# Performance work log

Measured on AMD Instinct MI355X. Metric: run time of the kernel, lower is better.

## Reference

```python
import jax, jax.numpy as jnp
import numpy as np

O = 128      # o_size
E = 512      # embed_dim
H = 128      # h_size
V = 34       # num_letter
B = 2048     # batch
T = 512      # listener timesteps
EPS = 1e-5   # BatchNorm eps


def _lstm_cell(x, h, c, W_ih, W_hh, b_ih, b_hh):
    # PyTorch LSTMCell: gates ordered i, f, g, o
    g = x @ W_ih.T + b_ih + h @ W_hh.T + b_hh
    i, f, gg, o = jnp.split(g, 4, axis=1)
    c_new = jax.nn.sigmoid(f) * c + jax.nn.sigmoid(i) * jnp.tanh(gg)
    h_new = jax.nn.sigmoid(o) * jnp.tanh(c_new)
    return h_new, c_new


def setup_inputs() -> dict:
    key = jax.random.key(0)
    ks = jax.random.split(key, 32)
    d = {}
    d['hk'] = jax.random.normal(ks[0], (B, T, O), jnp.float32)
    d['hv'] = jax.random.normal(ks[1], (B, T, O), jnp.float32)
    d['y_1'] = jax.random.normal(ks[2], (B, E), jnp.float32)
    d['c_1'] = jax.random.normal(ks[3], (B, O), jnp.float32)
    d['sh_1'] = jax.random.normal(ks[4], (3, B, O), jnp.float32)
    d['sc_1'] = jax.random.normal(ks[5], (3, B, O), jnp.float32)
    d['mask'] = jnp.ones((B, T), jnp.float32)
    s = 0.05
    in_dims = [O + E, O, O]
    for l in range(3):
        d[f'W_ih{l}'] = jax.random.normal(ks[6 + 4 * l], (4 * O, in_dims[l]), jnp.float32) * s
        d[f'W_hh{l}'] = jax.random.normal(ks[7 + 4 * l], (4 * O, O), jnp.float32) * s
        d[f'b_ih{l}'] = jax.random.normal(ks[8 + 4 * l], (4 * O,), jnp.float32) * s
        d[f'b_hh{l}'] = jax.random.normal(ks[9 + 4 * l], (4 * O,), jnp.float32) * s
    d['w1'] = jax.random.normal(ks[20], (H, O), jnp.float32) * s
    d['b1'] = jnp.zeros((H,), jnp.float32)
    d['w2'] = jax.random.normal(ks[21], (H, O), jnp.float32) * s
    d['b2'] = jnp.zeros((H,), jnp.float32)
    d['w3'] = jax.random.normal(ks[22], (V, H), jnp.float32) * s
    d['b3'] = jnp.zeros((V,), jnp.float32)
    d['gamma'] = jnp.ones((H,), jnp.float32)
    d['beta'] = jnp.zeros((H,), jnp.float32)
    return d


def reference(hk, hv, y_1, c_1, sh_1, sc_1, mask,
              W_ih0, W_hh0, b_ih0, b_hh0,
              W_ih1, W_hh1, b_ih1, b_hh1,
              W_ih2, W_hh2, b_ih2, b_hh2,
              w1, b1, w2, b2, w3, b3, gamma, beta):
    x0 = jnp.concatenate((y_1, c_1), axis=1)            # [B, E+O]
    sh0, sc0 = _lstm_cell(x0, sh_1[0], sc_1[0], W_ih0, W_hh0, b_ih0, b_hh0)
    sh1, sc1 = _lstm_cell(sh0, sh_1[1], sc_1[1], W_ih1, W_hh1, b_ih1, b_hh1)
    sh2, sc2 = _lstm_cell(sh1, sh_1[2], sc_1[2], W_ih2, W_hh2, b_ih2, b_hh2)

    # Attention: query is the CELL state sc2 (as in the original code)
    scores = jnp.einsum('bto,bo->bt', hk, sc2)           # [B, T]
    p = jax.nn.softmax(scores, axis=1)
    p = p * mask
    p = p / jnp.sum(p, axis=1, keepdims=True)            # mask-then-renormalize
    c = jnp.einsum('bt,bto->bo', p, hv)                  # [B, O]

    out = sh2 @ w1.T + b1 + (c @ w2.T + b2)              # [B, H]
    # BatchNorm1d (training mode: batch statistics, biased variance)
    mu = jnp.mean(out, axis=0)
    var = jnp.mean((out - mu) ** 2, axis=0)
    out = gamma * (out - mu) * jax.lax.rsqrt(var + EPS) + beta
    out = jax.nn.relu(out)
    out = out @ w3.T + b3                                # [B, V]
    out = jax.nn.softmax(out, axis=1)
    return out, c, jnp.stack([sh0, sh1, sh2]), jnp.stack([sc0, sc1, sc2])
```

## Files before the change

### kernel.cpp

```cpp
#include <hip/hip_runtime.h>
#include <hip/hip_bf16.h>

#define BSZ 2048
#define TSZ 512
#define OSZ 128
#define ESZ 512
#define HSZ 128
#define VSZ 34

#define OFF_C   69632
#define OFF_SH  331776
#define OFF_SC  1118208
#define LAYER   262144

__device__ __forceinline__ float sigf(float x)  { return 1.0f / (1.0f + __expf(-x)); }
__device__ __forceinline__ float tanhf_(float x){ return 2.0f / (1.0f + __expf(-2.0f * x)) - 1.0f; }

__global__ __launch_bounds__(256) void lstm_cell_kernel(
    const float* __restrict__ A0, int w0,
    const float* __restrict__ A1, int w1,
    const float* __restrict__ A2,
    const float* __restrict__ Wih, int in_dim,
    const float* __restrict__ Whh,
    const float* __restrict__ bih, const float* __restrict__ bhh,
    const float* __restrict__ c_prev,
    float* __restrict__ h_out, float* __restrict__ c_out,
    int K)
{
    __shared__ float As[16][68];
    __shared__ float Bs[16][68];

    const int tid = threadIdx.x;
    const int bm = blockIdx.x * 64;
    const int bn = blockIdx.y * 64;

    const int lRow = tid >> 2;
    const int lKq  = (tid & 3) * 4;

    const int nPerm = bn + (tid >> 2);
    const int nSrc  = (nPerm & 3) * 128 + (nPerm >> 2);

    const int tx = tid & 15, ty = tid >> 4;
    const int jT = (bn >> 2) + tx;

    float acc[4][4];
#pragma unroll
    for (int cc = 0; cc < 4; ++cc) {
        float bv = bih[cc * 128 + jT] + bhh[cc * 128 + jT];
#pragma unroll
        for (int r = 0; r < 4; ++r) acc[r][cc] = bv;
    }

    auto loadA = [&](int k0) -> float4 {
        int kg = k0 + lKq;
        const float* p;
        if (kg < w0)           p = A0 + (size_t)(bm + lRow) * w0 + kg;
        else if (kg < w0 + w1) p = A1 + (size_t)(bm + lRow) * w1 + (kg - w0);
        else                   p = A2 + (size_t)(bm + lRow) * 128 + (kg - w0 - w1);
        return *(const float4*)p;
    };
    auto loadB = [&](int k0) -> float4 {
        int kg = k0 + lKq;
        const float* p;
        if (kg < in_dim) p = Wih + (size_t)nSrc * in_dim + kg;
        else             p = Whh + (size_t)nSrc * 128 + (kg - in_dim);
        return *(const float4*)p;
    };

    float4 aR = loadA(0);
    float4 bR = loadB(0);
    const int ktiles = K >> 4;

    for (int kt = 0; kt < ktiles; ++kt) {
        As[lKq + 0][lRow] = aR.x; As[lKq + 1][lRow] = aR.y;
        As[lKq + 2][lRow] = aR.z; As[lKq + 3][lRow] = aR.w;
        Bs[lKq + 0][tid >> 2] = bR.x; Bs[lKq + 1][tid >> 2] = bR.y;
        Bs[lKq + 2][tid >> 2] = bR.z; Bs[lKq + 3][tid >> 2] = bR.w;
        __syncthreads();
        if (kt + 1 < ktiles) {
            aR = loadA((kt + 1) << 4);
            bR = loadB((kt + 1) << 4);
        }
#pragma unroll
        for (int k = 0; k < 16; ++k) {
            float4 av = *(const float4*)&As[k][ty * 4];
            float4 bv = *(const float4*)&Bs[k][tx * 4];
            float a_[4] = {av.x, av.y, av.z, av.w};
            float b_[4] = {bv.x, bv.y, bv.z, bv.w};
#pragma unroll
            for (int r = 0; r < 4; ++r)
#pragma unroll
                for (int c = 0; c < 4; ++c)
                    acc[r][c] += a_[r] * b_[c];
        }
        __syncthreads();
    }

#pragma unroll
    for (int r = 0; r < 4; ++r) {
        int row = bm + ty * 4 + r;
        float gi = acc[r][0], gf = acc[r][1], gg = acc[r][2], go = acc[r][3];
        float cp = c_prev[(size_t)row * 128 + jT];
        float cn = sigf(gf) * cp + sigf(gi) * tanhf_(gg);
        float hn = sigf(go) * tanhf_(cn);
        c_out[(size_t)row * 128 + jT] = cn;
        h_out[(size_t)row * 128 + jT] = hn;
    }
}

__global__ __launch_bounds__(256) void attn_kernel(
    const float* __restrict__ hk, const float* __restrict__ hv,
    const float* __restrict__ mask, const float* __restrict__ sc2,
    float* __restrict__ c_out)
{
    const int b = blockIdx.x;
    const int tid = threadIdx.x;
    __shared__ float sP[512];
    __shared__ float sRed[8];
    __shared__ float sC[8][128];

    const float* hkb = hk + (size_t)b * (TSZ * OSZ);
    const int og = (tid & 31) * 4;
    const int tg = tid >> 5;
    float4 q = *(const float4*)(sc2 + (size_t)b * 128 + og);

    for (int it = 0; it < 64; ++it) {
        float4 v = *(const float4*)(hkb + it * 1024 + tid * 4);
        float d = v.x * q.x + v.y * q.y + v.z * q.z + v.w * q.w;
        d += __shfl_xor(d, 1, 32);
        d += __shfl_xor(d, 2, 32);
        d += __shfl_xor(d, 4, 32);
        d += __shfl_xor(d, 8, 32);
        d += __shfl_xor(d, 16, 32);
        if ((tid & 31) == 0) sP[it * 8 + tg] = d;
    }
    __syncthreads();

    float m = fmaxf(sP[tid], sP[tid + 256]);
#pragma unroll
    for (int off = 1; off < 64; off <<= 1) m = fmaxf(m, __shfl_xor(m, off, 64));
    if ((tid & 63) == 0) sRed[tid >> 6] = m;
    __syncthreads();
    m = fmaxf(fmaxf(sRed[0], sRed[1]), fmaxf(sRed[2], sRed[3]));

    const float* mk = mask + (size_t)b * TSZ;
    float e0 = __expf(sP[tid] - m) * mk[tid];
    float e1 = __expf(sP[tid + 256] - m) * mk[tid + 256];
    float s = e0 + e1;
#pragma unroll
    for (int off = 1; off < 64; off <<= 1) s += __shfl_xor(s, off, 64);
    if ((tid & 63) == 0) sRed[4 + (tid >> 6)] = s;
    __syncthreads();
    float inv = 1.0f / (sRed[4] + sRed[5] + sRed[6] + sRed[7]);
    sP[tid]       = e0 * inv;
    sP[tid + 256] = e1 * inv;
    __syncthreads();

    float4 acc = {0.f, 0.f, 0.f, 0.f};
    const float* hvb = hv + (size_t)b * (TSZ * OSZ);
    for (int it = 0; it < 64; ++it) {
        float p = sP[it * 8 + tg];
        float4 v = *(const float4*)(hvb + it * 1024 + tid * 4);
        acc.x += p * v.x; acc.y += p * v.y; acc.z += p * v.z; acc.w += p * v.w;
    }
    *(float4*)&sC[tg][og] = acc;
    __syncthreads();
    if (tid < 128) {
        float r = 0.f;
#pragma unroll
        for (int g = 0; g < 8; ++g) r += sC[g][tid];
        c_out[(size_t)b * 128 + tid] = r;
    }
}

__global__ __launch_bounds__(256) void head_pre_kernel(
    const float* __restrict__ sh2, const float* __restrict__ cvec,
    const float* __restrict__ w1, const float* __restrict__ b1,
    const float* __restrict__ w2, const float* __restrict__ b2,
    float* __restrict__ out_pre, float* __restrict__ sum_part,
    float* __restrict__ sq_part)
{
    __shared__ float xs[8][128];
    __shared__ float xc[8][128];
    __shared__ float ps[2][128];
    __shared__ float pq[2][128];
    const int tid = threadIdx.x;
    const int rb = blockIdx.x * 8;
    {
        int row = tid >> 5, off = (tid & 31) * 4;
        *(float4*)&xs[row][off] = *(const float4*)(sh2 + (size_t)(rb + row) * 128 + off);
        *(float4*)&xc[row][off] = *(const float4*)(cvec + (size_t)(rb + row) * 128 + off);
    }
    __syncthreads();

    const int col = tid & 127, rg = tid >> 7;
    float acc[4];
    float bb = b1[col] + b2[col];
#pragma unroll
    for (int r = 0; r < 4; ++r) acc[r] = bb;
    const float* w1r = w1 + (size_t)col * 128;
    const float* w2r = w2 + (size_t)col * 128;
    for (int k4 = 0; k4 < 32; ++k4) {
        float4 wa = *(const float4*)(w1r + k4 * 4);
        float4 wb = *(const float4*)(w2r + k4 * 4);
#pragma unroll
        for (int r = 0; r < 4; ++r) {
            float4 xa = *(const float4*)&xs[rg * 4 + r][k4 * 4];
            float4 xb = *(const float4*)&xc[rg * 4 + r][k4 * 4];
            acc[r] += xa.x * wa.x + xa.y * wa.y + xa.z * wa.z + xa.w * wa.w
                    + xb.x * wb.x + xb.y * wb.y + xb.z * wb.z + xb.w * wb.w;
        }
    }
    float s = 0.f, q = 0.f;
#pragma unroll
    for (int r = 0; r < 4; ++r) {
        out_pre[(size_t)(rb + rg * 4 + r) * 128 + col] = acc[r];
        s += acc[r]; q += acc[r] * acc[r];
    }
    ps[rg][col] = s; pq[rg][col] = q;
    __syncthreads();
    if (rg == 0) {
        sum_part[blockIdx.x * 128 + col] = ps[0][col] + ps[1][col];
        sq_part[blockIdx.x * 128 + col]  = pq[0][col] + pq[1][col];
    }
}

__global__ __launch_bounds__(256) void bn_stats_kernel(
    const float* __restrict__ sum_part, const float* __restrict__ sq_part,
    float* __restrict__ mu_out, float* __restrict__ rstd_out)
{
    __shared__ float s2[2][128], q2[2][128];
    const int tid = threadIdx.x;
    const int col = tid & 127, h = tid >> 7;
    float s = 0.f, q = 0.f;
    for (int p = h * 128; p < h * 128 + 128; ++p) {
        s += sum_part[p * 128 + col];
        q += sq_part[p * 128 + col];
    }
    s2[h][col] = s; q2[h][col] = q;
    __syncthreads();
    if (h == 0) {
        float st = s2[0][col] + s2[1][col];
        float qt = q2[0][col] + q2[1][col];
        float mu = st * (1.0f / 2048.0f);
        float var = qt * (1.0f / 2048.0f) - mu * mu;
        mu_out[col] = mu;
        rstd_out[col] = rsqrtf(var + 1e-5f);
    }
}

__global__ __launch_bounds__(256) void head_post_kernel(
    const float* __restrict__ out_pre, const float* __restrict__ mu_buf,
    const float* __restrict__ rstd_buf, const float* __restrict__ gamma,
    const float* __restrict__ beta, const float* __restrict__ w3,
    const float* __restrict__ b3, float* __restrict__ out0)
{
    __shared__ float xn[8][128];
    __shared__ float lg[8][34];
    const int tid = threadIdx.x;
    const int rb = blockIdx.x * 8;
    {
        int row = tid >> 5, off = (tid & 31) * 4;
        float4 v   = *(const float4*)(out_pre + (size_t)(rb + row) * 128 + off);
        float4 mu4 = *(const float4*)(mu_buf + off);
        float4 rs4 = *(const float4*)(rstd_buf + off);
        float4 g4  = *(const float4*)(gamma + off);
        float4 b4  = *(const float4*)(beta + off);
        float4 o;
        o.x = fmaxf(g4.x * (v.x - mu4.x) * rs4.x + b4.x, 0.0f);
        o.y = fmaxf(g4.y * (v.y - mu4.y) * rs4.y + b4.y, 0.0f);
        o.z = fmaxf(g4.z * (v.z - mu4.z) * rs4.z + b4.z, 0.0f);
        o.w = fmaxf(g4.w * (v.w - mu4.w) * rs4.w + b4.w, 0.0f);
        *(float4*)&xn[row][off] = o;
    }
    __syncthreads();

    for (int idx = tid; idx < 8 * VSZ; idx += 256) {
        int row = idx / VSZ, vv = idx % VSZ;
        const float* w3r = w3 + (size_t)vv * 128;
        float acc = b3[vv];
        for (int k4 = 0; k4 < 32; ++k4) {
            float4 x4 = *(const float4*)&xn[row][k4 * 4];
            float4 wv = *(const float4*)(w3r + k4 * 4);
            acc += x4.x * wv.x + x4.y * wv.y + x4.z * wv.z + x4.w * wv.w;
        }
        lg[row][vv] = acc;
    }
    __syncthreads();

    const int row = tid >> 5, lane = tid & 31;
    float m = -1e30f;
    for (int vv = lane; vv < VSZ; vv += 32) m = fmaxf(m, lg[row][vv]);
#pragma unroll
    for (int off = 1; off < 32; off <<= 1) m = fmaxf(m, __shfl_xor(m, off, 32));
    float e0 = __expf(lg[row][lane] - m);
    float e1 = (lane + 32 < VSZ) ? __expf(lg[row][lane + 32] - m) : 0.0f;
    float s = e0 + e1;
#pragma unroll
    for (int off = 1; off < 32; off <<= 1) s += __shfl_xor(s, off, 32);
    float inv = 1.0f / s;
    out0[(size_t)(rb + row) * VSZ + lane] = e0 * inv;
    if (lane + 32 < VSZ) out0[(size_t)(rb + row) * VSZ + lane + 32] = e1 * inv;
}

extern "C" void kernel_launch(void* const* d_in, const int* in_sizes, int n_in,
                              void* d_out, int out_size, void* d_ws, size_t ws_size,
                              hipStream_t stream)
{
    const float* hk   = (const float*)d_in[0];
    const float* hv   = (const float*)d_in[1];
    const float* y_1  = (const float*)d_in[2];
    const float* c_1  = (const float*)d_in[3];
    const float* sh_1 = (const float*)d_in[4];
    const float* sc_1 = (const float*)d_in[5];
    const float* mask = (const float*)d_in[6];
    const float* Wih0 = (const float*)d_in[7];
    const float* Whh0 = (const float*)d_in[8];
    const float* bih0 = (const float*)d_in[9];
    const float* bhh0 = (const float*)d_in[10];
    const float* Wih1 = (const float*)d_in[11];
    const float* Whh1 = (const float*)d_in[12];
    const float* bih1 = (const float*)d_in[13];
    const float* bhh1 = (const float*)d_in[14];
    const float* Wih2 = (const float*)d_in[15];
    const float* Whh2 = (const float*)d_in[16];
    const float* bih2 = (const float*)d_in[17];
    const float* bhh2 = (const float*)d_in[18];
    const float* w1   = (const float*)d_in[19];
    const float* b1   = (const float*)d_in[20];
    const float* w2   = (const float*)d_in[21];
    const float* b2   = (const float*)d_in[22];
    const float* w3   = (const float*)d_in[23];
    const float* b3   = (const float*)d_in[24];
    const float* gamma= (const float*)d_in[25];
    const float* beta = (const float*)d_in[26];

    float* out   = (float*)d_out;
    float* outC  = out + OFF_C;
    float* outSH = out + OFF_SH;
    float* outSC = out + OFF_SC;

    float* ws       = (float*)d_ws;
    float* out_pre  = ws;
    float* sum_part = ws + 262144;
    float* sq_part  = sum_part + 32768;
    float* mu_buf   = sq_part + 32768;
    float* rstd_buf = mu_buf + 128;

    dim3 gG(32, 8), bG(256);
    lstm_cell_kernel<<<gG, bG, 0, stream>>>(
        y_1, 512, c_1, 128, sh_1, Wih0, 640, Whh0, bih0, bhh0,
        sc_1, outSH, outSC, 768);
    lstm_cell_kernel<<<gG, bG, 0, stream>>>(
        outSH, 128, nullptr, 0, sh_1 + LAYER, Wih1, 128, Whh1, bih1, bhh1,
        sc_1 + LAYER, outSH + LAYER, outSC + LAYER, 256);
    lstm_cell_kernel<<<gG, bG, 0, stream>>>(
        outSH + LAYER, 128, nullptr, 0, sh_1 + 2 * LAYER, Wih2, 128, Whh2, bih2, bhh2,
        sc_1 + 2 * LAYER, outSH + 2 * LAYER, outSC + 2 * LAYER, 256);
    attn_kernel<<<BSZ, 256, 0, stream>>>(hk, hv, mask, outSC + 2 * LAYER, outC);
    head_pre_kernel<<<256, 256, 0, stream>>>(outSH + 2 * LAYER, outC, w1, b1, w2, b2,
                                             out_pre, sum_part, sq_part);
    bn_stats_kernel<<<1, 256, 0, stream>>>(sum_part, sq_part, mu_buf, rstd_buf);
    head_post_kernel<<<256, 256, 0, stream>>>(out_pre, mu_buf, rstd_buf, gamma, beta,
                                              w3, b3, out);
}
```

Baseline: 306.1 us.

## Use bf16 MFMA for LSTM cell gate GEMMs

Replaces the fp32 SIMT register-tiled GEMM in the LSTM cell kernels with bf16 MFMA 16x16x32 instructions. Inputs and weights are converted to bf16 while staging into an XOR-swizzled LDS tile, and each wave computes the four gate tiles for 16 hidden units. This is meant to cut the compute time of the three gate GEMMs. In exchange, gate precision drops to bf16 inputs.

```diff
diff --git a/kernel.cpp b/kernel.cpp
--- a/kernel.cpp
+++ b/kernel.cpp
@@ -13,10 +13,19 @@
 #define OFF_SC  1118208
 #define LAYER   262144
 
+typedef __attribute__((ext_vector_type(8))) short s16x8;
+typedef __attribute__((ext_vector_type(4))) float f32x4;
+
 __device__ __forceinline__ float sigf(float x)  { return 1.0f / (1.0f + __expf(-x)); }
 __device__ __forceinline__ float tanhf_(float x){ return 2.0f / (1.0f + __expf(-2.0f * x)) - 1.0f; }
 
-__global__ __launch_bounds__(256) void lstm_cell_kernel(
+__device__ __forceinline__ short f2b(float f) {
+    return (short)__bfloat16_as_ushort(__float2bfloat16(f));
+}
+
+struct F8 { float4 lo, hi; };
+
+__global__ __launch_bounds__(256) void lstm_cell_mfma(
     const float* __restrict__ A0, int w0,
     const float* __restrict__ A1, int w1,
     const float* __restrict__ A2,
@@ -27,84 +36,83 @@
     float* __restrict__ h_out, float* __restrict__ c_out,
     int K)
 {
-    __shared__ float As[16][68];
-    __shared__ float Bs[16][68];
+    __shared__ short lsA[64 * 32];
+    __shared__ short lsB[64 * 32];
 
     const int tid = threadIdx.x;
     const int bm = blockIdx.x * 64;
-    const int bn = blockIdx.y * 64;
-
-    const int lRow = tid >> 2;
-    const int lKq  = (tid & 3) * 4;
-
-    const int nPerm = bn + (tid >> 2);
-    const int nSrc  = (nPerm & 3) * 128 + (nPerm >> 2);
-
-    const int tx = tid & 15, ty = tid >> 4;
-    const int jT = (bn >> 2) + tx;
-
-    float acc[4][4];
-#pragma unroll
-    for (int cc = 0; cc < 4; ++cc) {
-        float bv = bih[cc * 128 + jT] + bhh[cc * 128 + jT];
-#pragma unroll
-        for (int r = 0; r < 4; ++r) acc[r][cc] = bv;
-    }
-
-    auto loadA = [&](int k0) -> float4 {
-        int kg = k0 + lKq;
+    const int j0 = blockIdx.y * 16;
+
+    const int sRow = tid >> 2;
+    const int sKc  = (tid & 3) << 3;
+    const int sOff = sRow * 32 + ((((tid & 3)) ^ (sRow & 3)) << 3);
+
+    const int w_row = (sRow >> 4) * 128 + j0 + (sRow & 15);
+
+    const int wav = tid >> 6, lan = tid & 63;
+    const int fr  = lan & 15;
+    const int fkb = lan >> 4;
+    const int aOff = (wav * 16 + fr) * 32 + ((fkb ^ (fr & 3)) << 3);
+    const int bOffBase = fr * 32 + ((fkb ^ (fr & 3)) << 3);
+
+    const int j = j0 + fr;
+
+    f32x4 acc[4];
+#pragma unroll
+    for (int t = 0; t < 4; ++t) {
+        float bv = bih[t * 128 + j] + bhh[t * 128 + j];
+        acc[t] = (f32x4){bv, bv, bv, bv};
+    }
+
+    auto loadA = [&](int kt) -> F8 {
+        int kg = kt * 32 + sKc;
         const float* p;
-        if (kg < w0)           p = A0 + (size_t)(bm + lRow) * w0 + kg;
-        else if (kg < w0 + w1) p = A1 + (size_t)(bm + lRow) * w1 + (kg - w0);
-        else                   p = A2 + (size_t)(bm + lRow) * 128 + (kg - w0 - w1);
-        return *(const float4*)p;
+        if (kg < w0)           p = A0 + (size_t)(bm + sRow) * w0 + kg;
+        else if (kg < w0 + w1) p = A1 + (size_t)(bm + sRow) * w1 + (kg - w0);
+        else                   p = A2 + (size_t)(bm + sRow) * 128 + (kg - w0 - w1);
+        F8 r; r.lo = *(const float4*)p; r.hi = *(const float4*)(p + 4); return r;
     };
-    auto loadB = [&](int k0) -> float4 {
-        int kg = k0 + lKq;
+    auto loadB = [&](int kt) -> F8 {
+        int kg = kt * 32 + sKc;
         const float* p;
-        if (kg < in_dim) p = Wih + (size_t)nSrc * in_dim + kg;
-        else             p = Whh + (size_t)nSrc * 128 + (kg - in_dim);
-        return *(const float4*)p;
+        if (kg < in_dim) p = Wih + (size_t)w_row * in_dim + kg;
+        else             p = Whh + (size_t)w_row * 128 + (kg - in_dim);
+        F8 r; r.lo = *(const float4*)p; r.hi = *(const float4*)(p + 4); return r;
     };
 
-    float4 aR = loadA(0);
-    float4 bR = loadB(0);
-    const int ktiles = K >> 4;
-
-    for (int kt = 0; kt < ktiles; ++kt) {
-        As[lKq + 0][lRow] = aR.x; As[lKq + 1][lRow] = aR.y;
-        As[lKq + 2][lRow] = aR.z; As[lKq + 3][lRow] = aR.w;
-        Bs[lKq + 0][tid >> 2] = bR.x; Bs[lKq + 1][tid >> 2] = bR.y;
-        Bs[lKq + 2][tid >> 2] = bR.z; Bs[lKq + 3][tid >> 2] = bR.w;
+    const int nk = K >> 5;
+    F8 aV = loadA(0);
+    F8 bV = loadB(0);
+
+    for (int kt = 0; kt < nk; ++kt) {
+        s16x8 ap, bp;
+        ap[0] = f2b(aV.lo.x); ap[1] = f2b(aV.lo.y); ap[2] = f2b(aV.lo.z); ap[3] = f2b(aV.lo.w);
+        ap[4] = f2b(aV.hi.x); ap[5] = f2b(aV.hi.y); ap[6] = f2b(aV.hi.z); ap[7] = f2b(aV.hi.w);
+        bp[0] = f2b(bV.lo.x); bp[1] = f2b(bV.lo.y); bp[2] = f2b(bV.lo.z); bp[3] = f2b(bV.lo.w);
+        bp[4] = f2b(bV.hi.x); bp[5] = f2b(bV.hi.y); bp[6] = f2b(bV.hi.z); bp[7] = f2b(bV.hi.w);
+        *(s16x8*)(lsA + sOff) = ap;
+        *(s16x8*)(lsB + sOff) = bp;
         __syncthreads();
-        if (kt + 1 < ktiles) {
-            aR = loadA((kt + 1) << 4);
-            bR = loadB((kt + 1) << 4);
-        }
-#pragma unroll
-        for (int k = 0; k < 16; ++k) {
-            float4 av = *(const float4*)&As[k][ty * 4];
-            float4 bv = *(const float4*)&Bs[k][tx * 4];
-            float a_[4] = {av.x, av.y, av.z, av.w};
-            float b_[4] = {bv.x, bv.y, bv.z, bv.w};
-#pragma unroll
-            for (int r = 0; r < 4; ++r)
-#pragma unroll
-                for (int c = 0; c < 4; ++c)
-                    acc[r][c] += a_[r] * b_[c];
+        if (kt + 1 < nk) { aV = loadA(kt + 1); bV = loadB(kt + 1); }
+
+        s16x8 af = *(const s16x8*)(lsA + aOff);
+#pragma unroll
+        for (int t = 0; t < 4; ++t) {
+            s16x8 bf = *(const s16x8*)(lsB + bOffBase + t * 512);
+            acc[t] = __builtin_amdgcn_mfma_f32_16x16x32_bf16(af, bf, acc[t], 0, 0, 0);
         }
         __syncthreads();
     }
 
 #pragma unroll
     for (int r = 0; r < 4; ++r) {
-        int row = bm + ty * 4 + r;
-        float gi = acc[r][0], gf = acc[r][1], gg = acc[r][2], go = acc[r][3];
-        float cp = c_prev[(size_t)row * 128 + jT];
+        int row = bm + wav * 16 + fkb * 4 + r;
+        float gi = acc[0][r], gf = acc[1][r], gg = acc[2][r], go = acc[3][r];
+        float cp = c_prev[(size_t)row * 128 + j];
         float cn = sigf(gf) * cp + sigf(gi) * tanhf_(gg);
         float hn = sigf(go) * tanhf_(cn);
-        c_out[(size_t)row * 128 + jT] = cn;
-        h_out[(size_t)row * 128 + jT] = hn;
+        c_out[(size_t)row * 128 + j] = cn;
+        h_out[(size_t)row * 128 + j] = hn;
     }
 }
 
@@ -348,13 +356,13 @@
     float* rstd_buf = mu_buf + 128;
 
     dim3 gG(32, 8), bG(256);
-    lstm_cell_kernel<<<gG, bG, 0, stream>>>(
+    lstm_cell_mfma<<<gG, bG, 0, stream>>>(
         y_1, 512, c_1, 128, sh_1, Wih0, 640, Whh0, bih0, bhh0,
         sc_1, outSH, outSC, 768);
-    lstm_cell_kernel<<<gG, bG, 0, stream>>>(
+    lstm_cell_mfma<<<gG, bG, 0, stream>>>(
         outSH, 128, nullptr, 0, sh_1 + LAYER, Wih1, 128, Whh1, bih1, bhh1,
         sc_1 + LAYER, outSH + LAYER, outSC + LAYER, 256);
-    lstm_cell_kernel<<<gG, bG, 0, stream>>>(
+    lstm_cell_mfma<<<gG, bG, 0, stream>>>(
         outSH + LAYER, 128, nullptr, 0, sh_1 + 2 * LAYER, Wih2, 128, Whh2, bih2, bhh2,
         sc_1 + 2 * LAYER, outSH + 2 * LAYER, outSC + 2 * LAYER, 256);
     attn_kernel<<<BSZ, 256, 0, stream>>>(hk, hv, mask, outSC + 2 * LAYER, outC);
```

After: 277.7 us. 9.3% less time.
